# Optimization experiments

Hardware: AMD Instinct MI355X
Metric: run time of the kernel (lower is better)

Reference implementation:

```python
import jax, jax.numpy as jnp
import numpy as np

D_MODEL = 1024
N_HEAD = 16
D_HEAD = D_MODEL // N_HEAD
B, S = 4, 2048


def setup_inputs() -> dict:
    key = jax.random.key(0)
    ks = jax.random.split(key, 9)
    s = 1.0 / np.sqrt(D_MODEL)
    inp = {"x": jax.random.normal(ks[0], (B, S, D_MODEL), dtype=jnp.float32)}
    for i, name in enumerate(["q", "k", "v", "o"]):
        inp[f"W{name}"] = jax.random.uniform(ks[1 + 2 * i], (D_MODEL, D_MODEL), jnp.float32, -s, s)
        inp[f"b{name}"] = jax.random.uniform(ks[2 + 2 * i], (D_MODEL,), jnp.float32, -s, s)
    return inp


def reference(x, Wq, bq, Wk, bk, Wv, bv, Wo, bo):
    b, sq, _ = x.shape
    skv = sq
    # projections (torch Linear: x @ W^T + b), reshape to (b, h, s, d)
    def proj(W, bias):
        return (x @ W.T + bias).reshape(b, sq, N_HEAD, D_HEAD).transpose(0, 2, 1, 3)
    q, k, v = proj(Wq, bq), proj(Wk, bk), proj(Wv, bv)
    scale = np.sqrt(D_HEAD).astype(np.float32)
    scores = jnp.einsum("bhqd,bhkd->bhqk", q, k) / scale
    causal_mask = jnp.triu(jnp.ones((sq, skv), dtype=bool), k=1)
    scores = jnp.where(causal_mask, -jnp.inf, scores)
    attn = jax.nn.softmax(scores, axis=-1)
    o = jnp.einsum("bhqk,bhkd->bhqd", attn, v)  # (b, h, sq, d_head)
    o = o.transpose(0, 2, 1, 3).reshape(b, sq, D_MODEL)
    return o @ Wo.T + bo
```

## Files before the change

### kernel.cpp

```cpp
#include <hip/hip_runtime.h>
#include <hip/hip_bf16.h>
#include <math.h>

#define S_LEN 2048
#define DMODEL 1024
#define NHEAD 16
#define DHEAD 64
#define BATCH 4
#define MROWS (BATCH * S_LEN)

typedef unsigned short u16;
typedef __attribute__((ext_vector_type(4))) unsigned short u16x4;
typedef __attribute__((ext_vector_type(2))) unsigned u32x2;
typedef __attribute__((ext_vector_type(8))) short bf16x8;
typedef __attribute__((ext_vector_type(4))) float f32x4;

#define GLDS16(g, l)                                              \
  __builtin_amdgcn_global_load_lds(                               \
      (const __attribute__((address_space(1))) void*)(g),         \
      (__attribute__((address_space(3))) void*)(l), 16, 0, 0)

__device__ __forceinline__ u16 f2bf(float f) {
  unsigned u = __float_as_uint(f);
  u += 0x7fff + ((u >> 16) & 1);
  return (u16)(u >> 16);
}

__device__ __forceinline__ float exp2v(float x) {
  float r;
  asm("v_exp_f32 %0, %1" : "=v"(r) : "v"(x));
  return r;
}

__device__ __forceinline__ f32x4 mfma16(bf16x8 a, bf16x8 b, f32x4 c) {
  return __builtin_amdgcn_mfma_f32_16x16x32_bf16(a, b, c, 0, 0, 0);
}

__global__ __launch_bounds__(256) void castk(const float* __restrict__ in,
                                             u16* __restrict__ out, int n) {
  int i = (blockIdx.x * 256 + threadIdx.x) * 4;
  if (i >= n) return;
  f32x4 v = *(const f32x4*)(in + i);
  u16 a0 = f2bf(v[0]), a1 = f2bf(v[1]), a2 = f2bf(v[2]), a3 = f2bf(v[3]);
  out[i + 0] = a0; out[i + 1] = a1; out[i + 2] = a2; out[i + 3] = a3;
}

__global__ __launch_bounds__(256) void castw(
    const float* __restrict__ i0, const float* __restrict__ i1,
    const float* __restrict__ i2, const float* __restrict__ i3,
    u16* __restrict__ o0, u16* __restrict__ o1,
    u16* __restrict__ o2, u16* __restrict__ o3) {
  const int m = blockIdx.y;
  const float* in = m == 0 ? i0 : (m == 1 ? i1 : (m == 2 ? i2 : i3));
  u16* out = m == 0 ? o0 : (m == 1 ? o1 : (m == 2 ? o2 : o3));
  int i = (blockIdx.x * 256 + threadIdx.x) * 4;
  f32x4 v = *(const f32x4*)(in + i);
  u16 a0 = f2bf(v[0]), a1 = f2bf(v[1]), a2 = f2bf(v[2]), a3 = f2bf(v[3]);
  out[i + 0] = a0; out[i + 1] = a1; out[i + 2] = a2; out[i + 3] = a3;
}

__global__ __launch_bounds__(256) void gemm_qkv(
    const u16* __restrict__ Xb,
    const u16* __restrict__ W0, const u16* __restrict__ W1, const u16* __restrict__ W2,
    const float* __restrict__ b0, const float* __restrict__ b1, const float* __restrict__ b2,
    u16* __restrict__ O0, u16* __restrict__ O1, u16* __restrict__ O2) {
  __shared__ u16 As[128 * 64];
  __shared__ u16 Bs[128 * 64];
  const int flat = blockIdx.x;
  const int xcd = flat & 7, idx = flat >> 3;
  const int ymt = xcd * 8 + idx / 24;
  const int rem = idx % 24;
  const int xnt = rem & 7;
  const int z = rem >> 3;
  const u16* Wm = z == 0 ? W0 : (z == 1 ? W1 : W2);
  const float* bias = z == 0 ? b0 : (z == 1 ? b1 : b2);
  u16* Out = z == 0 ? O0 : (z == 1 ? O1 : O2);
  const float qs = (z == 0) ? 0.18033688011112042f : 1.0f;
  const int tid = threadIdx.x;
  const int wave = tid >> 6, lane = tid & 63, g = lane >> 4, c = lane & 15;
  const int wm = wave >> 1, wn = wave & 1;
  const int bm0 = ymt * 128, bn0 = xnt * 128;

  f32x4 acc[4][4];
#pragma unroll
  for (int m = 0; m < 4; ++m)
#pragma unroll
    for (int n = 0; n < 4; ++n) acc[m][n] = (f32x4){0.f, 0.f, 0.f, 0.f};

  for (int k0 = 0; k0 < DMODEL; k0 += 64) {
    __syncthreads();
#pragma unroll
    for (int cc = 0; cc < 4; ++cc) {
      const int ci = cc * 256 + tid;
      const int row = ci >> 3, ch = ci & 7;
      const int sc = ((ch ^ (row & 7)) << 3);
      GLDS16(Xb + (size_t)(bm0 + row) * DMODEL + k0 + sc,
             (char*)As + (cc * 256 + wave * 64) * 16);
      GLDS16(Wm + (size_t)(bn0 + row) * DMODEL + k0 + sc,
             (char*)Bs + (cc * 256 + wave * 64) * 16);
    }
    __syncthreads();
#pragma unroll
    for (int ks = 0; ks < 2; ++ks) {
      bf16x8 af[4], bfr[4];
#pragma unroll
      for (int m = 0; m < 4; ++m) {
        const int arow = wm * 64 + m * 16 + c;
        af[m] = *(const bf16x8*)((const char*)As + arow * 128 +
                                 (((ks * 4 + g) ^ (arow & 7)) << 4));
      }
#pragma unroll
      for (int n = 0; n < 4; ++n) {
        const int brow = wn * 64 + n * 16 + c;
        bfr[n] = *(const bf16x8*)((const char*)Bs + brow * 128 +
                                  (((ks * 4 + g) ^ (brow & 7)) << 4));
      }
#pragma unroll
      for (int m = 0; m < 4; ++m)
#pragma unroll
        for (int n = 0; n < 4; ++n)
          acc[m][n] = mfma16(af[m], bfr[n], acc[m][n]);
    }
  }
  if (z < 2) {
#pragma unroll
    for (int n = 0; n < 4; ++n) {
      const int coln = bn0 + wn * 64 + n * 16 + c;
      const float bn_ = bias[coln];
      const int h = coln >> 6, d = coln & 63;
#pragma unroll
      for (int m = 0; m < 4; ++m) {
#pragma unroll
        for (int r = 0; r < 4; ++r) {
          const int rowm = bm0 + wm * 64 + m * 16 + g * 4 + r;
          const int b_ = rowm >> 11, s_ = rowm & 2047;
          Out[(((size_t)(b_ * NHEAD + h) * S_LEN + s_) << 6) + d] =
              f2bf((acc[m][n][r] + bn_) * qs);
        }
      }
    }
  } else {
#pragma unroll
    for (int n = 0; n < 4; ++n) {
      const int coln = bn0 + wn * 64 + n * 16 + c;
      const float bn_ = bias[coln];
      const int h = coln >> 6, d = coln & 63;
#pragma unroll
      for (int m = 0; m < 4; ++m) {
        const int row0 = bm0 + wm * 64 + m * 16 + g * 4;
        const int b_ = row0 >> 11, s_ = row0 & 2047;
        u16x4 pk;
#pragma unroll
        for (int r = 0; r < 4; ++r) pk[r] = f2bf(acc[m][n][r] + bn_);
        *(u16x4*)(Out + ((size_t)(b_ * NHEAD + h) * DHEAD + d) * S_LEN + s_) = pk;
      }
    }
  }
}

__global__ __launch_bounds__(256) void gemm_out(
    const u16* __restrict__ Ab, const u16* __restrict__ Wm,
    const float* __restrict__ bias, float* __restrict__ Out) {
  __shared__ u16 As[128 * 64];
  __shared__ u16 Bs[128 * 64];
  const int flat = blockIdx.x;
  const int xcd = flat & 7, idx = flat >> 3;
  const int ymt = xcd * 8 + (idx >> 3);
  const int xnt = idx & 7;
  const int tid = threadIdx.x;
  const int wave = tid >> 6, lane = tid & 63, g = lane >> 4, c = lane & 15;
  const int wm = wave >> 1, wn = wave & 1;
  const int bm0 = ymt * 128, bn0 = xnt * 128;

  f32x4 acc[4][4];
#pragma unroll
  for (int m = 0; m < 4; ++m)
#pragma unroll
    for (int n = 0; n < 4; ++n) acc[m][n] = (f32x4){0.f, 0.f, 0.f, 0.f};

  for (int k0 = 0; k0 < DMODEL; k0 += 64) {
    __syncthreads();
#pragma unroll
    for (int cc = 0; cc < 4; ++cc) {
      const int ci = cc * 256 + tid;
      const int row = ci >> 3, ch = ci & 7;
      const int sc = ((ch ^ (row & 7)) << 3);
      GLDS16(Ab + (size_t)(bm0 + row) * DMODEL + k0 + sc,
             (char*)As + (cc * 256 + wave * 64) * 16);
      GLDS16(Wm + (size_t)(bn0 + row) * DMODEL + k0 + sc,
             (char*)Bs + (cc * 256 + wave * 64) * 16);
    }
    __syncthreads();
#pragma unroll
    for (int ks = 0; ks < 2; ++ks) {
      bf16x8 af[4], bfr[4];
#pragma unroll
      for (int m = 0; m < 4; ++m) {
        const int arow = wm * 64 + m * 16 + c;
        af[m] = *(const bf16x8*)((const char*)As + arow * 128 +
                                 (((ks * 4 + g) ^ (arow & 7)) << 4));
      }
#pragma unroll
      for (int n = 0; n < 4; ++n) {
        const int brow = wn * 64 + n * 16 + c;
        bfr[n] = *(const bf16x8*)((const char*)Bs + brow * 128 +
                                  (((ks * 4 + g) ^ (brow & 7)) << 4));
      }
#pragma unroll
      for (int m = 0; m < 4; ++m)
#pragma unroll
        for (int n = 0; n < 4; ++n)
          acc[m][n] = mfma16(af[m], bfr[n], acc[m][n]);
    }
  }
#pragma unroll
  for (int n = 0; n < 4; ++n) {
    const int coln = bn0 + wn * 64 + n * 16 + c;
    const float bn_ = bias[coln];
#pragma unroll
    for (int m = 0; m < 4; ++m) {
#pragma unroll
      for (int r = 0; r < 4; ++r) {
        const int rowm = bm0 + wm * 64 + m * 16 + g * 4 + r;
        Out[(size_t)rowm * DMODEL + coln] = acc[m][n][r] + bn_;
      }
    }
  }
}

__global__ __launch_bounds__(256) void attn_fwd(const u16* __restrict__ Qb,
                                                const u16* __restrict__ Kb,
                                                const u16* __restrict__ VTb,
                                                u16* __restrict__ AOb) {
  __shared__ u16 Kt[64 * 64];
  __shared__ u16 Vt[64 * 64];
  __shared__ unsigned Pl[4][16 * 36];
  const int tid = threadIdx.x;
  const int w = tid >> 6, lane = tid & 63, g = lane >> 4, c = lane & 15;
  const int flat = blockIdx.x;
  const int wg = (flat & 7) * 128 + (flat >> 3);
  const int bh = wg >> 4;
  const int pr = wg & 15;
  const size_t base = (size_t)bh * (S_LEN * DHEAD);
  const int b_ = bh >> 4, h = bh & 15;
  const int ci0 = w * 64 + lane;

#pragma unroll
  for (int pass = 0; pass < 2; ++pass) {
    const int qt = pass ? pr : (31 - pr);
    const int qb = qt * 64;
    const int q = qb + w * 16 + c;
    const bf16x8 qf0 = *(const bf16x8*)(Qb + base + (size_t)q * 64 + g * 8);
    const bf16x8 qf1 = *(const bf16x8*)(Qb + base + (size_t)q * 64 + 32 + g * 8);

    f32x4 oacc[4];
#pragma unroll
    for (int dt = 0; dt < 4; ++dt) oacc[dt] = (f32x4){0.f, 0.f, 0.f, 0.f};
    float m = -30000.f, l = 0.f;

    const int nt = qt + 1;
    for (int kt = 0; kt < nt; ++kt) {
      const int kv0 = kt * 64;
      __syncthreads();
#pragma unroll
      for (int call = 0; call < 2; ++call) {
        const int ci = call * 256 + ci0;
        const int row = ci >> 3;
        const int colg = (ci & 7) ^ (row & 7);
        GLDS16(Kb + base + (size_t)(kv0 + row) * 64 + colg * 8,
               (char*)Kt + (call * 256 + w * 64) * 16);
        GLDS16(VTb + base + (size_t)row * S_LEN + kv0 + colg * 8,
               (char*)Vt + (call * 256 + w * 64) * 16);
      }
      __syncthreads();

      f32x4 s[4];
#pragma unroll
      for (int t = 0; t < 4; ++t) {
        const int krow = t * 16 + c;
        const char* kbase = (const char*)Kt + krow * 128;
        bf16x8 kf0 = *(const bf16x8*)(kbase + ((g ^ (krow & 7)) * 16));
        bf16x8 kf1 = *(const bf16x8*)(kbase + (((4 + g) ^ (krow & 7)) * 16));
        f32x4 zacc = (f32x4){0.f, 0.f, 0.f, 0.f};
        zacc = mfma16(kf0, qf0, zacc);
        zacc = mfma16(kf1, qf1, zacc);
        s[t] = zacc;
      }
      if (kt == nt - 1) {
#pragma unroll
        for (int t = 0; t < 4; ++t)
#pragma unroll
          for (int r = 0; r < 4; ++r)
            if (kv0 + t * 16 + 4 * g + r > q) s[t][r] = -30000.f;
      }
      const float a0 = fmaxf(fmaxf(s[0][0], s[0][1]), s[0][2]);
      const float a1 = fmaxf(fmaxf(s[0][3], s[1][0]), s[1][1]);
      const float a2 = fmaxf(fmaxf(s[1][2], s[1][3]), s[2][0]);
      const float a3 = fmaxf(fmaxf(s[2][1], s[2][2]), s[2][3]);
      const float a4 = fmaxf(fmaxf(s[3][0], s[3][1]), s[3][2]);
      float pm = fmaxf(fmaxf(fmaxf(a0, a1), a2), fmaxf(fmaxf(a3, a4), s[3][3]));
      pm = fmaxf(pm, __shfl_xor(pm, 16));
      pm = fmaxf(pm, __shfl_xor(pm, 32));
      if (__any(pm > m + 8.0f)) {
        const float mn = fmaxf(m, pm);
        const float sc = exp2v(m - mn);
        l *= sc;
#pragma unroll
        for (int dt = 0; dt < 4; ++dt) oacc[dt] *= sc;
        m = mn;
      }
      float rs = 0.f;
#pragma unroll
      for (int t = 0; t < 4; ++t) {
        const float p0 = exp2v(s[t][0] - m), p1 = exp2v(s[t][1] - m);
        const float p2 = exp2v(s[t][2] - m), p3 = exp2v(s[t][3] - m);
        rs += (p0 + p1) + (p2 + p3);
        const unsigned b0 = __float_as_uint(p0) + 0x8000u;
        const unsigned b1 = __float_as_uint(p1) + 0x8000u;
        const unsigned b2 = __float_as_uint(p2) + 0x8000u;
        const unsigned b3 = __float_as_uint(p3) + 0x8000u;
        u32x2 pk2;
        pk2[0] = __builtin_amdgcn_perm(b1, b0, 0x07060302u);
        pk2[1] = __builtin_amdgcn_perm(b3, b2, 0x07060302u);
        *(u32x2*)&Pl[w][c * 36 + t * 8 + g * 2] = pk2;
      }
      rs += __shfl_xor(rs, 16);
      rs += __shfl_xor(rs, 32);
      l += rs;

#pragma unroll
      for (int kk = 0; kk < 2; ++kk) {
        const bf16x8 pb = *(const bf16x8*)&Pl[w][c * 36 + kk * 16 + g * 4];
#pragma unroll
        for (int dt = 0; dt < 4; ++dt) {
          const int vrow = dt * 16 + c;
          const bf16x8 vf = *(const bf16x8*)((const char*)Vt + vrow * 128 +
                                             (((kk * 4 + g) ^ (vrow & 7)) * 16));
          oacc[dt] = mfma16(vf, pb, oacc[dt]);
        }
      }
    }
    const float inv = 1.0f / l;
    const size_t rowbase = ((size_t)(b_ * S_LEN + q) * DMODEL) + h * 64;
#pragma unroll
    for (int dt = 0; dt < 4; ++dt) {
      u16x4 pk4;
#pragma unroll
      for (int r = 0; r < 4; ++r) pk4[r] = f2bf(oacc[dt][r] * inv);
      *(u16x4*)(AOb + rowbase + dt * 16 + 4 * g) = pk4;
    }
  }
}

extern "C" void kernel_launch(void* const* d_in, const int* in_sizes, int n_in,
                              void* d_out, int out_size, void* d_ws, size_t ws_size,
                              hipStream_t stream) {
  const float* x  = (const float*)d_in[0];
  const float* Wq = (const float*)d_in[1];
  const float* bq = (const float*)d_in[2];
  const float* Wk = (const float*)d_in[3];
  const float* bk = (const float*)d_in[4];
  const float* Wv = (const float*)d_in[5];
  const float* bv = (const float*)d_in[6];
  const float* Wo = (const float*)d_in[7];
  const float* bo = (const float*)d_in[8];
  float* out = (float*)d_out;
  char* ws = (char*)d_ws;

  const size_t MB = 1024 * 1024;
  u16* xb  = (u16*)(ws);
  u16* Wqb = (u16*)(ws + 16 * MB);
  u16* Wkb = (u16*)(ws + 18 * MB);
  u16* Wvb = (u16*)(ws + 20 * MB);
  u16* Wob = (u16*)(ws + 22 * MB);
  u16* Qb  = (u16*)(ws + 24 * MB);
  u16* Kb  = (u16*)(ws + 40 * MB);
  u16* VTb = (u16*)(ws + 56 * MB);
  u16* AOb = (u16*)(ws + 72 * MB);

  castk<<<8192, 256, 0, stream>>>(x, xb, MROWS * DMODEL);
  castw<<<dim3(1024, 4), 256, 0, stream>>>(Wq, Wk, Wv, Wo, Wqb, Wkb, Wvb, Wob);

  gemm_qkv<<<1536, 256, 0, stream>>>(
      xb, Wqb, Wkb, Wvb, bq, bk, bv, Qb, Kb, VTb);

  attn_fwd<<<1024, 256, 0, stream>>>(Qb, Kb, VTb, AOb);

  gemm_out<<<512, 256, 0, stream>>>(AOb, Wob, bo, out);
}
```

Measured before the change: 179.0 us.

## Double-buffer K/V tiles in attention and pass P via lane shuffles

The attention kernel now keeps two LDS buffers for K and V and issues the next tile's global-to-LDS loads before computing on the current one, using explicit vmcnt waits and raw barriers instead of two __syncthreads per tile. It also drops the per-wave LDS staging of the bf16 probability matrix, rebuilding the MFMA B-operand with cross-lane shuffles instead. This is meant to hide K/V load latency and remove an LDS round trip. The costs are double the K/V LDS footprint, which may lower occupancy, and extra shuffle instructions. The hand-written vmcnt count and the barrier placement must also stay correct.

```diff
diff --git a/kernel.cpp b/kernel.cpp
--- a/kernel.cpp
+++ b/kernel.cpp
@@ -232,11 +232,13 @@
                                                 const u16* __restrict__ Kb,
                                                 const u16* __restrict__ VTb,
                                                 u16* __restrict__ AOb) {
-  __shared__ u16 Kt[64 * 64];
-  __shared__ u16 Vt[64 * 64];
-  __shared__ unsigned Pl[4][16 * 36];
+  __shared__ u16 Kt[2][64 * 64];
+  __shared__ u16 Vt[2][64 * 64];
   const int tid = threadIdx.x;
   const int w = tid >> 6, lane = tid & 63, g = lane >> 4, c = lane & 15;
+  const int ghi = g >> 1;
+  const int srcA = ((g & 1) << 5) + c;
+  const int srcB = srcA + 16;
   const int flat = blockIdx.x;
   const int wg = (flat & 7) * 128 + (flat >> 3);
   const int bh = wg >> 4;
@@ -245,6 +247,20 @@
   const int b_ = bh >> 4, h = bh & 15;
   const int ci0 = w * 64 + lane;
 
+#define STAGE(buf_, kt_) do {                                              \
+    const int kv0_ = (kt_) * 64;                                           \
+    _Pragma("unroll")                                                      \
+    for (int call = 0; call < 2; ++call) {                                 \
+      const int ci = call * 256 + ci0;                                     \
+      const int row_ = ci >> 3;                                            \
+      const int colg = (ci & 7) ^ (row_ & 7);                              \
+      GLDS16(Kb + base + (size_t)(kv0_ + row_) * 64 + colg * 8,            \
+             (char*)Kt[buf_] + (call * 256 + w * 64) * 16);                \
+      GLDS16(VTb + base + (size_t)row_ * S_LEN + kv0_ + colg * 8,          \
+             (char*)Vt[buf_] + (call * 256 + w * 64) * 16);                \
+    }                                                                      \
+  } while (0)
+
 #pragma unroll
   for (int pass = 0; pass < 2; ++pass) {
     const int qt = pass ? pr : (31 - pr);
@@ -259,26 +275,23 @@
     float m = -30000.f, l = 0.f;
 
     const int nt = qt + 1;
+    STAGE(0, 0);
     for (int kt = 0; kt < nt; ++kt) {
       const int kv0 = kt * 64;
-      __syncthreads();
-#pragma unroll
-      for (int call = 0; call < 2; ++call) {
-        const int ci = call * 256 + ci0;
-        const int row = ci >> 3;
-        const int colg = (ci & 7) ^ (row & 7);
-        GLDS16(Kb + base + (size_t)(kv0 + row) * 64 + colg * 8,
-               (char*)Kt + (call * 256 + w * 64) * 16);
-        GLDS16(VTb + base + (size_t)row * S_LEN + kv0 + colg * 8,
-               (char*)Vt + (call * 256 + w * 64) * 16);
-      }
-      __syncthreads();
+      const int cur = kt & 1;
+      if (kt + 1 < nt) {
+        STAGE((kt + 1) & 1, kt + 1);
+        asm volatile("s_waitcnt vmcnt(4)" ::: "memory");
+      } else {
+        asm volatile("s_waitcnt vmcnt(0)" ::: "memory");
+      }
+      __builtin_amdgcn_s_barrier();
 
       f32x4 s[4];
 #pragma unroll
       for (int t = 0; t < 4; ++t) {
         const int krow = t * 16 + c;
-        const char* kbase = (const char*)Kt + krow * 128;
+        const char* kbase = (const char*)Kt[cur] + krow * 128;
         bf16x8 kf0 = *(const bf16x8*)(kbase + ((g ^ (krow & 7)) * 16));
         bf16x8 kf1 = *(const bf16x8*)(kbase + (((4 + g) ^ (krow & 7)) * 16));
         f32x4 zacc = (f32x4){0.f, 0.f, 0.f, 0.f};
@@ -310,19 +323,18 @@
         m = mn;
       }
       float rs = 0.f;
+      unsigned pk[4][2];
 #pragma unroll
       for (int t = 0; t < 4; ++t) {
         const float p0 = exp2v(s[t][0] - m), p1 = exp2v(s[t][1] - m);
         const float p2 = exp2v(s[t][2] - m), p3 = exp2v(s[t][3] - m);
         rs += (p0 + p1) + (p2 + p3);
-        const unsigned b0 = __float_as_uint(p0) + 0x8000u;
-        const unsigned b1 = __float_as_uint(p1) + 0x8000u;
-        const unsigned b2 = __float_as_uint(p2) + 0x8000u;
-        const unsigned b3 = __float_as_uint(p3) + 0x8000u;
-        u32x2 pk2;
-        pk2[0] = __builtin_amdgcn_perm(b1, b0, 0x07060302u);
-        pk2[1] = __builtin_amdgcn_perm(b3, b2, 0x07060302u);
-        *(u32x2*)&Pl[w][c * 36 + t * 8 + g * 2] = pk2;
+        const unsigned q0 = __float_as_uint(p0) + 0x8000u;
+        const unsigned q1 = __float_as_uint(p1) + 0x8000u;
+        const unsigned q2 = __float_as_uint(p2) + 0x8000u;
+        const unsigned q3 = __float_as_uint(p3) + 0x8000u;
+        pk[t][0] = __builtin_amdgcn_perm(q1, q0, 0x07060302u);
+        pk[t][1] = __builtin_amdgcn_perm(q3, q2, 0x07060302u);
       }
       rs += __shfl_xor(rs, 16);
       rs += __shfl_xor(rs, 32);
@@ -330,15 +342,25 @@
 
 #pragma unroll
       for (int kk = 0; kk < 2; ++kk) {
-        const bf16x8 pb = *(const bf16x8*)&Pl[w][c * 36 + kk * 16 + g * 4];
+        union { int u[4]; bf16x8 v; } pb;
+#pragma unroll
+        for (int hh = 0; hh < 2; ++hh) {
+          const int eA = __shfl((int)pk[2 * kk][hh], srcA);
+          const int oA = __shfl((int)pk[2 * kk + 1][hh], srcA);
+          const int eB = __shfl((int)pk[2 * kk][hh], srcB);
+          const int oB = __shfl((int)pk[2 * kk + 1][hh], srcB);
+          pb.u[hh] = ghi ? oA : eA;
+          pb.u[2 + hh] = ghi ? oB : eB;
+        }
 #pragma unroll
         for (int dt = 0; dt < 4; ++dt) {
           const int vrow = dt * 16 + c;
-          const bf16x8 vf = *(const bf16x8*)((const char*)Vt + vrow * 128 +
+          const bf16x8 vf = *(const bf16x8*)((const char*)Vt[cur] + vrow * 128 +
                                              (((kk * 4 + g) ^ (vrow & 7)) * 16));
-          oacc[dt] = mfma16(vf, pb, oacc[dt]);
+          oacc[dt] = mfma16(vf, pb.v, oacc[dt]);
         }
       }
+      __builtin_amdgcn_s_barrier();
     }
     const float inv = 1.0f / l;
     const size_t rowbase = ((size_t)(b_ * S_LEN + q) * DMODEL) + h * 64;
@@ -350,6 +372,7 @@
       *(u16x4*)(AOb + rowbase + dt * 16 + 4 * g) = pk4;
     }
   }
+#undef STAGE
 }
 
 extern "C" void kernel_launch(void* const* d_in, const int* in_sizes, int n_in,
```

Result: slower. 188.0 us (+5.0%).
